# Optimization experiments

Measured on AMD Instinct MI355X. Metric: run time of the kernel, lower is better.

Reference implementation:

```python
import jax, jax.numpy as jnp
import numpy as np

H = 16  # num_heads

def _toroidal_bias(S, dtype):
    # float mask: +1.0 at (i, (i-1)%S), (i,i), (i, (i+1)%S); PyTorch ADDS float attn_mask to scores
    eye = jnp.eye(S, dtype=dtype)
    return eye + jnp.roll(eye, 1, axis=1) + jnp.roll(eye, -1, axis=1)

def setup_inputs() -> dict:
    key = jax.random.key(0)
    ks = jax.random.split(key, 7)
    E = 1024
    S, B = 2048, 2
    sc = 0.02
    return {
        "x": jax.random.normal(ks[0], (S, B, E), dtype=jnp.float32),
        "w_tor": jax.random.normal(ks[1], (E, E), dtype=jnp.float32) * sc,
        "b_tor": jax.random.normal(ks[2], (E,), dtype=jnp.float32) * sc,
        "in_proj_w": jax.random.normal(ks[3], (3 * E, E), dtype=jnp.float32) * sc,
        "in_proj_b": jax.random.normal(ks[4], (3 * E,), dtype=jnp.float32) * sc,
        "out_w": jax.random.normal(ks[5], (E, E), dtype=jnp.float32) * sc,
        "out_b": jax.random.normal(ks[6], (E,), dtype=jnp.float32) * sc,
    }

def reference(x, w_tor, b_tor, in_proj_w, in_proj_b, out_w, out_b):
    S, B, E = x.shape
    hd = E // H
    scale = 1.0 / jnp.sqrt(jnp.asarray(hd, dtype=x.dtype))
    # toroidal projection, then fused in_proj (self-attention: q=k=v=x_toroidal)
    xt = x @ w_tor.T + b_tor                      # (S,B,E)
    qkv = xt @ in_proj_w.T + in_proj_b            # (S,B,3E)
    q, k, v = jnp.split(qkv, 3, axis=-1)
    def to_heads(t):
        return t.reshape(S, B, H, hd).transpose(1, 2, 0, 3)  # (B,H,S,hd)
    q, k, v = to_heads(q), to_heads(k), to_heads(v)
    bias = _toroidal_bias(S, x.dtype)             # (S,S) additive float mask
    scores = jnp.einsum('bhqd,bhkd->bhqk', q * scale, k) + bias
    attn = jax.nn.softmax(scores, axis=-1)
    o = jnp.einsum('bhqk,bhkd->bhqd', attn, v)    # (B,H,S,hd)
    o = o.transpose(2, 0, 1, 3).reshape(S, B, E)
    return o @ out_w.T + out_b
```

## Files before the change

kernel.cpp:

```cpp
#include <hip/hip_runtime.h>

#define S_LEN 2048
#define NB    2
#define EMB   1024
#define NH    16
#define HD    64

typedef __bf16 bf16_t;
typedef bf16_t bf16x8 __attribute__((ext_vector_type(8)));
typedef bf16_t bf16x4v __attribute__((ext_vector_type(4)));
typedef float  f32x4  __attribute__((ext_vector_type(4)));
typedef float  f32x16 __attribute__((ext_vector_type(16)));

#define L2E 1.44269504f

__device__ __forceinline__ void g2l16(const void* g, void* l) {
    auto gp = reinterpret_cast<const unsigned int __attribute__((address_space(1)))*>(
        reinterpret_cast<uintptr_t>(g));
    auto lp = reinterpret_cast<unsigned int __attribute__((address_space(3)))*>(
        reinterpret_cast<uintptr_t>(l));
    __builtin_amdgcn_global_load_lds(gp, lp, 16, 0, 0);
}

__device__ __forceinline__ unsigned int pk2(float a, float b) {
    union { unsigned int u; bf16_t h[2]; } r;
    r.h[0] = (bf16_t)a; r.h[1] = (bf16_t)b;
    return r.u;
}

__global__ __launch_bounds__(256) void cast4_f32_bf16(
    const float* __restrict__ s0, bf16_t* __restrict__ d0,
    const float* __restrict__ s1, bf16_t* __restrict__ d1,
    const float* __restrict__ s2, bf16_t* __restrict__ d2,
    const float* __restrict__ s3, bf16_t* __restrict__ d3)
{
    long i = (long)blockIdx.x * 256 + threadIdx.x;
    const float* s; bf16_t* d; long off;
    if (i < 1048576)      { s = s0; d = d0; off = i; }
    else if (i < 1310720) { s = s1; d = d1; off = i - 1048576; }
    else if (i < 2097152) { s = s2; d = d2; off = i - 1310720; }
    else                  { s = s3; d = d3; off = i - 2097152; }
    float4 v = ((const float4*)s)[off];
    bf16x4v o;
    o[0] = (bf16_t)v.x; o[1] = (bf16_t)v.y; o[2] = (bf16_t)v.z; o[3] = (bf16_t)v.w;
    *(bf16x4v*)(d + off * 4) = o;
}

template<int TN, int MODE, int MT, int NT>
__global__ __launch_bounds__(256, 2) void gemm_bt_bf16(
    const bf16_t* __restrict__ A, const bf16_t* __restrict__ W,
    const float* __restrict__ bias, void* __restrict__ Cout,
    bf16_t* __restrict__ Qp, bf16_t* __restrict__ Kp, bf16_t* __restrict__ Vtp,
    int M, int N, int K)
{
    constexpr int MB  = (TN == 64) ? 2 : 4;
    constexpr int NBn = (TN == 64) ? 4 : TN / 32;
    constexpr int BI  = TN / 64;
    extern __shared__ __align__(16) char smem[];
    bf16_t* AsB = (bf16_t*)smem;
    bf16_t* BsB = (bf16_t*)(smem + 32768);

    const int tid  = threadIdx.x;
    const int lane = tid & 63;
    const int w    = tid >> 6;
    const int lm   = lane & 15;
    const int lq   = lane >> 4;

    constexpr int MR = MT / 4;
    constexpr int NR = NT / 2;
    const int bid  = blockIdx.x;
    const int xcd  = bid & 7;
    const int idx  = bid >> 3;
    const long m0  = (long)((xcd >> 1) * MR + idx / NR) * 128;
    const long n0  = (long)((xcd & 1) * NR + idx % NR) * TN;

    const int wm0  = (TN == 64) ? w * 32 : (w >> 1) * 64;
    const int wn0  = (TN == 64) ? 0 : (w & 1) * (TN / 2);

    f32x4 acc[MB][NBn];
#pragma unroll
    for (int i = 0; i < MB; ++i)
#pragma unroll
        for (int j = 0; j < NBn; ++j) acc[i][j] = (f32x4){0.f, 0.f, 0.f, 0.f};

    auto stage = [&](int t, int buf) {
        const int k0 = t * 64;
        bf16_t* asb = AsB + buf * 8192;
#pragma unroll
        for (int j = 0; j < 4; ++j) {
            int kh = j >> 1, jj = j & 1;
            int a   = (w * 2 + jj) * 64 + lane;
            int row = a >> 2;
            int c   = (a & 3) ^ ((row >> 1) & 3);
            g2l16(A + (m0 + row) * K + k0 + kh * 32 + c * 8,
                  asb + kh * 4096 + (w * 2 + jj) * 512);
        }
        bf16_t* bsb = BsB + buf * (TN * 64);
#pragma unroll
        for (int j = 0; j < 2 * BI; ++j) {
            int kh = j / BI, jj = j % BI;
            int a   = (w * BI + jj) * 64 + lane;
            int row = a >> 2;
            int c   = (a & 3) ^ ((row >> 1) & 3);
            g2l16(W + (n0 + row) * K + k0 + kh * 32 + c * 8,
                  bsb + kh * (TN * 32) + (w * BI + jj) * 512);
        }
    };

    stage(0, 0);
    const int NTILES = K / 64;
    for (int t = 0; t < NTILES; ++t) {
        const int cur = t & 1;
        asm volatile("s_waitcnt vmcnt(0)" ::: "memory");
        __syncthreads();
        if (t + 1 < NTILES) stage(t + 1, cur ^ 1);

#pragma unroll
        for (int kh = 0; kh < 2; ++kh) {
            const bf16_t* Ab = AsB + cur * 8192 + kh * 4096;
            const bf16_t* Bb = BsB + cur * (TN * 64) + kh * (TN * 32);
            bf16x8 af[MB], bfr[NBn];
#pragma unroll
            for (int mb = 0; mb < MB; ++mb) {
                int r = wm0 + mb * 16 + lm;
                af[mb] = *(const bf16x8*)&Ab[r * 32 + ((lq ^ ((r >> 1) & 3)) << 3)];
            }
#pragma unroll
            for (int nb = 0; nb < NBn; ++nb) {
                int r = wn0 + nb * 16 + lm;
                bfr[nb] = *(const bf16x8*)&Bb[r * 32 + ((lq ^ ((r >> 1) & 3)) << 3)];
            }
#pragma unroll
            for (int mb = 0; mb < MB; ++mb)
#pragma unroll
                for (int nb = 0; nb < NBn; ++nb)
                    acc[mb][nb] = __builtin_amdgcn_mfma_f32_16x16x32_bf16(
                        af[mb], bfr[nb], acc[mb][nb], 0, 0, 0);
        }
    }

    float b4[NBn];
#pragma unroll
    for (int nb = 0; nb < NBn; ++nb) b4[nb] = bias[n0 + wn0 + nb * 16 + lm];

    if (MODE == 2) {
#pragma unroll
        for (int mb = 0; mb < MB; ++mb) {
            const long mbase = m0 + wm0 + mb * 16 + lq * 4;
#pragma unroll
            for (int nb = 0; nb < NBn; ++nb) {
                int n    = (int)n0 + wn0 + nb * 16 + lm;
                int sec  = n >> 10;
                int nloc = n & 1023;
                int h    = nloc >> 6;
                int d    = nloc & 63;
                if (sec == 2) {
                    int s0 = (int)(mbase >> 1);
                    int sp = (s0 & ~12) | ((s0 & 4) << 1) | ((s0 & 8) >> 1);
#pragma unroll
                    for (int rp = 0; rp < 2; ++rp) {
                        int bh = rp * 16 + h;
                        unsigned int pkv = pk2(acc[mb][nb][rp]     + b4[nb],
                                               acc[mb][nb][rp + 2] + b4[nb]);
                        *(unsigned int*)&Vtp[((size_t)(bh * 64 + d)) * S_LEN + sp] = pkv;
                    }
                } else {
#pragma unroll
                    for (int r = 0; r < 4; ++r) {
                        long m  = mbase + r;
                        int  s  = (int)(m >> 1), b = (int)(m & 1);
                        int  bh = b * 16 + h;
                        float v = acc[mb][nb][r] + b4[nb];
                        if (sec == 0) {
                            Qp[((size_t)(bh * S_LEN + s)) * 64 + d] =
                                (bf16_t)(v * (0.125f * L2E));
                        } else {
                            Kp[((size_t)(bh * S_LEN + s)) * 64 + d] = (bf16_t)v;
                        }
                    }
                }
            }
        }
    } else {
#pragma unroll
        for (int mb = 0; mb < MB; ++mb) {
#pragma unroll
            for (int r = 0; r < 4; ++r) {
                long m = m0 + wm0 + mb * 16 + lq * 4 + r;
#pragma unroll
                for (int nb = 0; nb < NBn; ++nb) {
                    int n   = (int)n0 + wn0 + nb * 16 + lm;
                    float v = acc[mb][nb][r] + b4[nb];
                    if (MODE == 0) ((float*)Cout)[m * N + n] = v;
                    else           ((bf16_t*)Cout)[m * N + n] = (bf16_t)v;
                }
            }
        }
    }
}

__global__ __launch_bounds__(256, 2) void attn_mfma(
    const bf16_t* __restrict__ Qb, const bf16_t* __restrict__ Kb,
    const bf16_t* __restrict__ Vtb, bf16_t* __restrict__ O)
{
    __shared__ __align__(16) bf16_t Ks[2][8 * 512];
    __shared__ __align__(16) bf16_t Vts[2][8 * 512];
    __shared__ __align__(16) float  Lw4[4][32];

    const int tid  = threadIdx.x;
    const int lane = tid & 63;
    const int w    = tid >> 6;
    const int bid  = blockIdx.x;
    const int bh   = ((bid & 7) << 2) | (bid >> 7);
    const int qt   = (bid >> 3) & 15;
    const int l5   = lane & 31;
    const int hi   = lane >> 5;

    const int rsub = lane >> 3;
    const int csw  = (lane & 7) ^ rsub;
    int cc[4];
#pragma unroll
    for (int i = 0; i < 4; ++i) cc[i] = ((2 * i + hi) ^ (l5 & 7)) * 8;

    const bf16_t* qrow = Qb + ((size_t)bh * S_LEN + qt * 128 + w * 32 + l5) * 64 + hi * 8;
    bf16x8 qf[4];
#pragma unroll
    for (int ds = 0; ds < 4; ++ds) qf[ds] = *(const bf16x8*)(qrow + ds * 16);

    f32x16 oacc[2];
#pragma unroll
    for (int dh = 0; dh < 2; ++dh)
#pragma unroll
        for (int i = 0; i < 16; ++i) oacc[dh][i] = 0.f;
    float plsum = 0.f;

    auto stageKV = [&](int kt, int buf) {
        bf16_t* ksb = &Ks[buf][0];
        bf16_t* vsb = &Vts[buf][0];
        const bf16_t* kg = Kb + ((size_t)bh * S_LEN + kt * 64) * 64;
        const bf16_t* vg = Vtb + (size_t)bh * 64 * S_LEN + kt * 64;
#pragma unroll
        for (int j = 0; j < 2; ++j) {
            int i = w * 2 + j;
            g2l16(kg + (size_t)(i * 8 + rsub) * 64 + csw * 8,    ksb + i * 512);
            g2l16(vg + (size_t)(i * 8 + rsub) * S_LEN + csw * 8, vsb + i * 512);
        }
    };

    stageKV(0, 0);
    for (int kt = 0; kt < 32; ++kt) {
        const int cur = kt & 1;
        asm volatile("s_waitcnt vmcnt(0)" ::: "memory");
        __syncthreads();
        if (kt < 31) stageKV(kt + 1, cur ^ 1);

        f32x16 sacc[2];
        __builtin_amdgcn_s_setprio(1);
#pragma unroll
        for (int kh = 0; kh < 2; ++kh) {
#pragma unroll
            for (int i = 0; i < 16; ++i) sacc[kh][i] = 0.f;
#pragma unroll
            for (int ds = 0; ds < 4; ++ds) {
                bf16x8 kf = *(const bf16x8*)&Ks[cur][(kh * 32 + l5) * 64 + cc[ds]];
                sacc[kh] = __builtin_amdgcn_mfma_f32_32x32x16_bf16(kf, qf[ds], sacc[kh], 0, 0, 0);
            }
        }
        __builtin_amdgcn_s_setprio(0);

        int ktd = (kt - 2 * qt) & 31;
        if (ktd <= 2 || ktd == 31) {
            int q = qt * 128 + w * 32 + l5;
#pragma unroll
            for (int kh = 0; kh < 2; ++kh)
#pragma unroll
                for (int r = 0; r < 16; ++r) {
                    int key  = kt * 64 + kh * 32 + (r & 3) + 8 * (r >> 2) + 4 * hi;
                    int diff = (key - q) & (S_LEN - 1);
                    if (diff <= 1 || diff == S_LEN - 1) sacc[kh][r] += L2E;
                }
        }

        float pv[2][16];
#pragma unroll
        for (int kh = 0; kh < 2; ++kh)
#pragma unroll
            for (int i = 0; i < 16; ++i) {
                pv[kh][i] = __builtin_amdgcn_exp2f(sacc[kh][i]);
                plsum += pv[kh][i];
            }

        bf16x8 pf[4];
#pragma unroll
        for (int ks = 0; ks < 4; ++ks) {
            const int kh = ks >> 1, m = ks & 1;
#pragma unroll
            for (int e = 0; e < 8; ++e)
                pf[ks][e] = (bf16_t)pv[kh][(e & 3) + 8 * m + 4 * (e >> 2)];
        }

        __builtin_amdgcn_s_setprio(1);
#pragma unroll
        for (int dh = 0; dh < 2; ++dh) {
#pragma unroll
            for (int ks = 0; ks < 4; ++ks) {
                bf16x8 vf = *(const bf16x8*)&Vts[cur][(dh * 32 + l5) * 64 + cc[ks]];
                oacc[dh] = __builtin_amdgcn_mfma_f32_32x32x16_bf16(pf[ks], vf, oacc[dh], 0, 0, 0);
            }
        }
        __builtin_amdgcn_s_setprio(0);
    }

    plsum += __shfl_xor(plsum, 32, 64);
    if (hi == 0) Lw4[w][l5] = plsum;

    float inv16[16];
#pragma unroll
    for (int g = 0; g < 4; ++g) {
        f32x4 lv = *(const f32x4*)&Lw4[w][8 * g + 4 * hi];
#pragma unroll
        for (int e = 0; e < 4; ++e) inv16[g * 4 + e] = 1.0f / lv[e];
    }

    const int b = bh >> 4, h = bh & 15;
#pragma unroll
    for (int dh = 0; dh < 2; ++dh)
#pragma unroll
        for (int r = 0; r < 16; ++r) {
            int qrel = (r & 3) + 8 * (r >> 2) + 4 * hi;
            int s = qt * 128 + w * 32 + qrel;
            O[((size_t)(s * NB + b)) * EMB + h * 64 + dh * 32 + l5] =
                (bf16_t)(oacc[dh][r] * inv16[r]);
        }
}

extern "C" void kernel_launch(void* const* d_in, const int* in_sizes, int n_in,
                              void* d_out, int out_size, void* d_ws, size_t ws_size,
                              hipStream_t stream)
{
    const float* x         = (const float*)d_in[0];
    const float* w_tor     = (const float*)d_in[1];
    const float* b_tor     = (const float*)d_in[2];
    const float* in_proj_w = (const float*)d_in[3];
    const float* in_proj_b = (const float*)d_in[4];
    const float* out_w     = (const float*)d_in[5];
    const float* out_b     = (const float*)d_in[6];
    float* out = (float*)d_out;

    const int M = S_LEN * NB;

    char* base = (char*)d_ws;
    bf16_t* xb    = (bf16_t*)(base);
    bf16_t* wtorb = (bf16_t*)(base + ( 8ull << 20));
    bf16_t* ipwb  = (bf16_t*)(base + (10ull << 20));
    bf16_t* outwb = (bf16_t*)(base + (16ull << 20));
    bf16_t* xtb   = (bf16_t*)(base + (18ull << 20));
    bf16_t* Kb    = (bf16_t*)(base + (26ull << 20));
    bf16_t* Vtb   = (bf16_t*)(base + (34ull << 20));
    bf16_t* Qb    = xb;
    bf16_t* Ob    = xtb;

    const int lds64  = 32768 + 64 * 256;
    const int lds192 = 32768 + 192 * 256;
    hipFuncSetAttribute((const void*)gemm_bt_bf16<192, 2, 32, 16>,
                        hipFuncAttributeMaxDynamicSharedMemorySize, lds192);

    cast4_f32_bf16<<<dim3(9216), 256, 0, stream>>>(
        x, xb, w_tor, wtorb, in_proj_w, ipwb, out_w, outwb);

    gemm_bt_bf16<64, 1, 32, 16><<<dim3(512), 256, lds64, stream>>>(
        xb, wtorb, b_tor, xtb, nullptr, nullptr, nullptr, M, EMB, EMB);

    gemm_bt_bf16<192, 2, 32, 16><<<dim3(512), 256, lds192, stream>>>(
        xtb, ipwb, in_proj_b, nullptr, Qb, Kb, Vtb, M, 3 * EMB, EMB);

    attn_mfma<<<dim3(32 * 16), 256, 0, stream>>>(Qb, Kb, Vtb, Ob);

    gemm_bt_bf16<64, 0, 32, 16><<<dim3(512), 256, lds64, stream>>>(
        Ob, outwb, out_b, out, nullptr, nullptr, nullptr, M, EMB, EMB);
}
```

Measured before the change: 196.8 us.

## Triple-buffer LDS staging in TN=64 GEMMs and attention K/V loads

The TN=64 GEMM variants and the attention kernel move from double to triple buffering of LDS tiles. Each loop iteration now prefetches two tiles ahead and waits only for the older loads with a partial vmcnt instead of draining all outstanding loads. The goal is to hide global-to-LDS latency behind MFMA work. The cost is more shared memory per block (72KB for the GEMM, 48KB for attention), which could lower occupancy. Correctness depends on the vmcnt thresholds matching the number of loads issued per stage.

```diff
diff --git a/kernel.cpp b/kernel.cpp
--- a/kernel.cpp
+++ b/kernel.cpp
@@ -53,12 +53,13 @@
     bf16_t* __restrict__ Qp, bf16_t* __restrict__ Kp, bf16_t* __restrict__ Vtp,
     int M, int N, int K)
 {
-    constexpr int MB  = (TN == 64) ? 2 : 4;
-    constexpr int NBn = (TN == 64) ? 4 : TN / 32;
-    constexpr int BI  = TN / 64;
+    constexpr int MB   = (TN == 64) ? 2 : 4;
+    constexpr int NBn  = (TN == 64) ? 4 : TN / 32;
+    constexpr int BI   = TN / 64;
+    constexpr int NBUF = (TN == 64) ? 3 : 2;
     extern __shared__ __align__(16) char smem[];
     bf16_t* AsB = (bf16_t*)smem;
-    bf16_t* BsB = (bf16_t*)(smem + 32768);
+    bf16_t* BsB = (bf16_t*)(smem + NBUF * 16384);
 
     const int tid  = threadIdx.x;
     const int lane = tid & 63;
@@ -107,13 +108,23 @@
         }
     };
 
+    const int NTILES = K / 64;
     stage(0, 0);
-    const int NTILES = K / 64;
+    if (NBUF == 3) stage(1, 1);
     for (int t = 0; t < NTILES; ++t) {
-        const int cur = t & 1;
-        asm volatile("s_waitcnt vmcnt(0)" ::: "memory");
+        const int cur = t % NBUF;
+        if (NBUF == 3) {
+            if (t + 1 < NTILES) asm volatile("s_waitcnt vmcnt(6)" ::: "memory");
+            else                asm volatile("s_waitcnt vmcnt(0)" ::: "memory");
+        } else {
+            asm volatile("s_waitcnt vmcnt(0)" ::: "memory");
+        }
         __syncthreads();
-        if (t + 1 < NTILES) stage(t + 1, cur ^ 1);
+        if (NBUF == 3) {
+            if (t + 2 < NTILES) stage(t + 2, (t + 2) % NBUF);
+        } else {
+            if (t + 1 < NTILES) stage(t + 1, (t + 1) % NBUF);
+        }
 
 #pragma unroll
         for (int kh = 0; kh < 2; ++kh) {
@@ -203,8 +214,8 @@
     const bf16_t* __restrict__ Qb, const bf16_t* __restrict__ Kb,
     const bf16_t* __restrict__ Vtb, bf16_t* __restrict__ O)
 {
-    __shared__ __align__(16) bf16_t Ks[2][8 * 512];
-    __shared__ __align__(16) bf16_t Vts[2][8 * 512];
+    __shared__ __align__(16) bf16_t Ks[3][8 * 512];
+    __shared__ __align__(16) bf16_t Vts[3][8 * 512];
     __shared__ __align__(16) float  Lw4[4][32];
 
     const int tid  = threadIdx.x;
@@ -248,11 +259,13 @@
     };
 
     stageKV(0, 0);
+    stageKV(1, 1);
     for (int kt = 0; kt < 32; ++kt) {
-        const int cur = kt & 1;
-        asm volatile("s_waitcnt vmcnt(0)" ::: "memory");
+        const int cur = kt % 3;
+        if (kt + 1 < 32) asm volatile("s_waitcnt vmcnt(4)" ::: "memory");
+        else             asm volatile("s_waitcnt vmcnt(0)" ::: "memory");
         __syncthreads();
-        if (kt < 31) stageKV(kt + 1, cur ^ 1);
+        if (kt + 2 < 32) stageKV(kt + 2, (kt + 2) % 3);
 
         f32x16 sacc[2];
         __builtin_amdgcn_s_setprio(1);
@@ -360,8 +373,12 @@
     bf16_t* Qb    = xb;
     bf16_t* Ob    = xtb;
 
-    const int lds64  = 32768 + 64 * 256;
-    const int lds192 = 32768 + 192 * 256;
+    const int lds64  = 3 * (16384 + 8192);
+    const int lds192 = 2 * (16384 + 24576);
+    hipFuncSetAttribute((const void*)gemm_bt_bf16<64, 1, 32, 16>,
+                        hipFuncAttributeMaxDynamicSharedMemorySize, lds64);
+    hipFuncSetAttribute((const void*)gemm_bt_bf16<64, 0, 32, 16>,
+                        hipFuncAttributeMaxDynamicSharedMemorySize, lds64);
     hipFuncSetAttribute((const void*)gemm_bt_bf16<192, 2, 32, 16>,
                         hipFuncAttributeMaxDynamicSharedMemorySize, lds192);
 
```

New measurement: 199.4 us. No clear change (+1.3%).
